# Kernel optimization log

Measured on AMD Instinct MI355X. Metric: run time of the kernel, lower is better.

The kernel has to match this reference:

```python
import math
import jax, jax.numpy as jnp
import numpy as np

N_HEADS = 16

def _alibi_slopes(n_heads: int) -> np.ndarray:
    def pow2_slopes(n):
        start = 2 ** (-2 ** (-(math.log2(n) - 3)))
        return [start * start ** i for i in range(n)]
    if math.log2(n_heads).is_integer():
        slopes = pow2_slopes(n_heads)
    else:
        closest = 2 ** math.floor(math.log2(n_heads))
        slopes = pow2_slopes(closest)
        extra = pow2_slopes(2 * closest)[0::2]
        slopes = slopes + extra[: n_heads - closest]
    return np.asarray(slopes, dtype=np.float32)

def _build_alibi_bias(n_heads: int, T: int) -> jnp.ndarray:
    # (1, H, T, T): lower triangle = -slope*|i-j|, strict upper = -inf (causal)
    slopes = jnp.asarray(_alibi_slopes(n_heads))  # (H,)
    pos = jnp.arange(T)
    dist = pos[None, :] - pos[None, :].T  # (T, T), j - i
    causal = dist < 0  # future positions (j > i means dist>0? note: dist = j - i transposed)
    # match torch: distances = positions[None,:] - positions[:,None] -> dist[i,j] = j - i
    dist = pos[None, :] - pos[:, None]
    causal = dist > 0  # wait: torch masks distances < 0 where distances[i,j] = j - i? No:
    # torch: distances = positions.unsqueeze(0) - positions.unsqueeze(1) -> dist[i,j] = positions[j] - positions[i]? 
    # unsqueeze(0): (1,T) row j; unsqueeze(1): (T,1) row i -> dist[i,j] = pos[j] - pos[i]
    # causal_mask = dist < 0 masks j < i ... but then bias upper triangle kept?
    # Actually torch masks where distances < 0, i.e., j < i (past). That seems inverted,
    # but we must be FAITHFUL: mask fills -inf where pos[j] - pos[i] < 0.
    d = pos[None, :] - pos[:, None]  # d[i,j] = j - i
    mask = d < 0
    bias = -slopes[:, None, None] * jnp.abs(d).astype(jnp.float32)[None, :, :]
    bias = jnp.where(mask[None, :, :], -jnp.inf, bias)
    return bias[None]  # (1, H, T, T)

def setup_inputs() -> dict:
    key = jax.random.key(0)
    k1, k2, k3 = jax.random.split(key, 3)
    B, T, D = 2, 2048, 1024
    x = jax.random.normal(k1, (B, T, D), dtype=jnp.float32)
    W_qkv = jax.random.normal(k2, (D, 3 * D), dtype=jnp.float32) * (1.0 / math.sqrt(D))
    W_out = jax.random.normal(k3, (D, D), dtype=jnp.float32) * (1.0 / math.sqrt(D))
    return {"x": x, "W_qkv": W_qkv, "W_out": W_out}

def reference(x, W_qkv, W_out):
    B, T, D = x.shape
    H = N_HEADS
    hd = D // H
    qkv = x @ W_qkv  # (B, T, 3D)
    q, k, v = jnp.split(qkv, 3, axis=-1)
    q = q.reshape(B, T, H, hd).transpose(0, 2, 1, 3)  # (B,H,T,hd)
    k = k.reshape(B, T, H, hd).transpose(0, 2, 1, 3)
    v = v.reshape(B, T, H, hd).transpose(0, 2, 1, 3)
    scale = 1.0 / math.sqrt(hd)
    attn = jnp.einsum('bhqd,bhkd->bhqk', q, k) * scale  # (B,H,T,T)
    attn = attn + _build_alibi_bias(H, T)
    attn = jax.nn.softmax(attn, axis=-1)
    out = jnp.einsum('bhqk,bhkd->bhqd', attn, v)  # (B,H,T,hd)
    out = out.transpose(0, 2, 1, 3).reshape(B, T, D)
    return out @ W_out
```

## Files before the change

kernel.cpp:

```cpp
#include <hip/hip_runtime.h>

#define DEV __device__ __forceinline__

typedef __attribute__((ext_vector_type(4))) float f32x4;
typedef __attribute__((ext_vector_type(16))) float f32x16;
typedef __attribute__((ext_vector_type(8))) short s16x8;

static constexpr int TB  = 2;
static constexpr int TT  = 2048;
static constexpr int TD  = 1024;
static constexpr int TH  = 16;
static constexpr int THD = 64;
static constexpr int TN3 = 3072;
static constexpr int TM  = TB * TT;

#define WS_FLAG   0u
#define WS_XB     1024u
#define WS_WQKVT  (WS_XB + 8388608u)
#define WS_WOUTT  (WS_WQKVT + 6291456u)
#define WS_QKV    (WS_WOUTT + 2097152u)
#define WS_VT     (WS_QKV + 25165824u)
#define WS_CTX    (WS_VT + 8388608u)

DEV unsigned short f2bf(float f) {
  unsigned int u = __builtin_bit_cast(unsigned int, f);
  u += 0x7FFFu + ((u >> 16) & 1u);
  return (unsigned short)(u >> 16);
}
DEV f32x4 mfma16(s16x8 a, s16x8 b, f32x4 c) {
  return __builtin_amdgcn_mfma_f32_16x16x32_bf16(a, b, c, 0, 0, 0);
}
DEV f32x16 mfma32(s16x8 a, s16x8 b, f32x16 c) {
  return __builtin_amdgcn_mfma_f32_32x32x16_bf16(a, b, c, 0, 0, 0);
}
DEV void gload_lds16(const void* g, void* l) {
  __builtin_amdgcn_global_load_lds(
      (const __attribute__((address_space(1))) void*)g,
      (__attribute__((address_space(3))) void*)l, 16, 0, 0);
}
DEV unsigned int cvtpk(float lo, float hi_) {
  unsigned int r;
  asm("v_cvt_pk_bf16_f32 %0, %1, %2" : "=v"(r) : "v"(lo), "v"(hi_));
  return r;
}
DEV void plswap(unsigned int& a, unsigned int& b) {
  asm("v_permlane32_swap_b32 %0, %1" : "+v"(a), "+v"(b));
}

__global__ __launch_bounds__(256) void detect_kernel(const uint4* __restrict__ probe,
                                                     int* __restrict__ flag) {
  __shared__ int cnt;
  if (threadIdx.x == 0) cnt = 0;
  __syncthreads();
  uint4 v = probe[threadIdx.x];
  int local = 0;
  unsigned int w[4] = {v.x, v.y, v.z, v.w};
#pragma unroll
  for (int k = 0; k < 4; ++k) {
    unsigned int e0 = (w[k] >> 7) & 0xFF;
    unsigned int e1 = (w[k] >> 23) & 0xFF;
    if (e0 >= 135) local++;
    if (e1 >= 135) local++;
  }
  atomicAdd(&cnt, local);
  __syncthreads();
  if (threadIdx.x == 0) flag[0] = (cnt < 100) ? 1 : 0;
}

__global__ __launch_bounds__(256) void prep_kernel(const void* __restrict__ x,
                                                   const void* __restrict__ wqkv,
                                                   const void* __restrict__ wout,
                                                   unsigned short* __restrict__ xb,
                                                   unsigned short* __restrict__ wqkvt,
                                                   unsigned short* __restrict__ woutt,
                                                   const int* __restrict__ flag) {
  __shared__ unsigned short tile[64 * 65];
  const int bid = blockIdx.x;
  const bool bf = (flag[0] != 0);
  if (bid < 1024) {
    const void* W; unsigned short* Wt; int N, k0, n0;
    if (bid < 768) { W = wqkv; Wt = wqkvt; N = TN3; k0 = (bid & 15) * 64; n0 = (bid >> 4) * 64; }
    else { int id = bid - 768; W = wout; Wt = woutt; N = TD; k0 = (id & 15) * 64; n0 = (id >> 4) * 64; }
    for (int e = threadIdx.x; e < 4096; e += 256) {
      int kr = e >> 6, nc = e & 63;
      unsigned short v;
      if (bf) v = ((const unsigned short*)W)[(size_t)(k0 + kr) * N + n0 + nc];
      else    v = f2bf(((const float*)W)[(size_t)(k0 + kr) * N + n0 + nc]);
      tile[kr * 65 + nc] = v;
    }
    __syncthreads();
    for (int e = threadIdx.x; e < 4096; e += 256) {
      int nr = e >> 6, kc = e & 63;
      Wt[(size_t)(n0 + nr) * TD + k0 + kc] = tile[kc * 65 + nr];
    }
  } else {
    if (bf) return;
    int i = (bid - 1024) * 256 + threadIdx.x;
    if (i >= (TM * TD) / 8) return;
    const float* s = (const float*)x + (size_t)i * 8;
    unsigned int w0 = (unsigned int)f2bf(s[0]) | ((unsigned int)f2bf(s[1]) << 16);
    unsigned int w1 = (unsigned int)f2bf(s[2]) | ((unsigned int)f2bf(s[3]) << 16);
    unsigned int w2 = (unsigned int)f2bf(s[4]) | ((unsigned int)f2bf(s[5]) << 16);
    unsigned int w3 = (unsigned int)f2bf(s[6]) | ((unsigned int)f2bf(s[7]) << 16);
    uint4 o; o.x = w0; o.y = w1; o.z = w2; o.w = w3;
    ((uint4*)xb)[i] = o;
  }
}

__global__ __launch_bounds__(512, 4) void gemm_8p_kernel(const unsigned short* __restrict__ Axb,
                                                         const unsigned short* __restrict__ xraw,
                                                         const unsigned short* __restrict__ Bt,
                                                         unsigned short* __restrict__ C,
                                                         unsigned short* __restrict__ vtb,
                                                         int Mn, int Nn, int Kn,
                                                         const int* __restrict__ flag) {
  __shared__ unsigned short lA[2][128 * 64];
  __shared__ unsigned short lB[2][192 * 64];
  const int tid = threadIdx.x;
  const int lane = tid & 63;
  const int wid = tid >> 6;
  const int wm = wid >> 2, wn = wid & 3;
  const int l15 = lane & 15, lg = lane >> 4;

  const int nby = Nn / 192;
  const int nwg = (Mn >> 7) * nby;
  const int cpx = nwg >> 3;
  const int bid = blockIdx.x;
  const int swz = (bid & 7) * cpx + (bid >> 3);
  const int bm = swz / nby, bn = swz % nby;
  const int row0 = bm << 7, col0 = bn * 192;

  const unsigned short* Abase = flag[0] ? xraw : Axb;

  const int srow = tid >> 3;
  const int scol = ((tid & 7) ^ (srow & 7)) * 8;
  const unsigned short* aS = Abase + (size_t)(row0 + srow) * Kn + scol;
  const unsigned short* bS = Bt + (size_t)(col0 + srow) * Kn + scol;
  const size_t r64 = (size_t)64 * Kn;

#define STGA(dst, koff) do {                                \
    unsigned short* _d = (dst) + tid * 8;                   \
    const unsigned short* _s = aS + (koff);                 \
    gload_lds16(_s,       _d);                              \
    gload_lds16(_s + r64, _d + 4096);                       \
  } while (0)
#define STGB(dst, koff) do {                                \
    unsigned short* _d = (dst) + tid * 8;                   \
    const unsigned short* _s = bS + (koff);                 \
    gload_lds16(_s,           _d);                          \
    gload_lds16(_s + r64,     _d + 4096);                   \
    gload_lds16(_s + 2 * r64, _d + 8192);                   \
  } while (0)

  f32x4 acc[4][3];
#pragma unroll
  for (int m = 0; m < 4; ++m)
#pragma unroll
    for (int n = 0; n < 3; ++n) acc[m][n] = (f32x4){0.f, 0.f, 0.f, 0.f};

  const int sa = l15 & 7;
  const int kc0 = (lg ^ sa) * 8;
  const int kc1 = ((4 + lg) ^ sa) * 8;
  const int aRow = (wm * 64 + l15) * 64;
  const int bRow = (wn * 48 + l15) * 64;

  STGA(&lA[0][0], 0);
  STGB(&lB[0][0], 0);
  asm volatile("s_waitcnt vmcnt(0)" ::: "memory");
  __builtin_amdgcn_s_barrier();

  const int nt = Kn >> 6;
  for (int t = 0; t < nt; ++t) {
    const unsigned short* la = &lA[t & 1][0];
    const unsigned short* lb = &lB[t & 1][0];
    unsigned short* na = &lA[(t + 1) & 1][0];
    unsigned short* nb = &lB[(t + 1) & 1][0];
    const int koff = (t + 1) << 6;
    const bool more = (t + 1 < nt);

    if (more) { STGA(na, koff); STGB(nb, koff); }

    s16x8 a0[4], a1[4], b0[3], b1[3];
#pragma unroll
    for (int m = 0; m < 4; ++m) {
      a0[m] = *(const s16x8*)&la[aRow + m * 1024 + kc0];
      a1[m] = *(const s16x8*)&la[aRow + m * 1024 + kc1];
    }
#pragma unroll
    for (int n = 0; n < 3; ++n) {
      b0[n] = *(const s16x8*)&lb[bRow + n * 1024 + kc0];
      b1[n] = *(const s16x8*)&lb[bRow + n * 1024 + kc1];
    }
#pragma unroll
    for (int m = 0; m < 4; ++m)
#pragma unroll
      for (int n = 0; n < 3; ++n) {
        acc[m][n] = mfma16(a0[m], b0[n], acc[m][n]);
        acc[m][n] = mfma16(a1[m], b1[n], acc[m][n]);
      }

    asm volatile("s_waitcnt vmcnt(0)" ::: "memory");
    __builtin_amdgcn_s_barrier();
  }
#undef STGA
#undef STGB

  unsigned short* cw = C + (size_t)(row0 + wm * 64 + lg * 4) * Nn + col0 + wn * 48 + l15;
#pragma unroll
  for (int m = 0; m < 4; ++m)
#pragma unroll
    for (int n = 0; n < 3; ++n) {
      const int cbase = col0 + wn * 48 + n * 16;
      if (cbase < 2048) {
#pragma unroll
        for (int j = 0; j < 4; ++j)
          cw[(size_t)(m * 16 + j) * Nn + n * 16] = f2bf(acc[m][n][j]);
      } else {
        int tg = row0 + wm * 64 + lg * 4 + m * 16;
        int bb = tg >> 11, tt = tg & 2047;
        int cc2 = cbase + l15 - 2048;
        int h = cc2 >> 6, d = cc2 & 63;
        unsigned short* dst = vtb + (((size_t)(bb * 16 + h) * 64 + d) << 11) + tt;
        uint2 pk;
        pk.x = cvtpk(acc[m][n][0], acc[m][n][1]);
        pk.y = cvtpk(acc[m][n][2], acc[m][n][3]);
        *(uint2*)dst = pk;
      }
    }
}

__global__ __launch_bounds__(256, 2) void gemm_bt2_kernel(const unsigned short* __restrict__ A,
                                                          const unsigned short* __restrict__ Bt,
                                                          void* __restrict__ Cout,
                                                          int Mn, int Nn, int Kn,
                                                          const int* __restrict__ flag) {
  __shared__ unsigned short lA[3][128 * 64];
  __shared__ unsigned short lB[3][64 * 64];
  const int tid  = threadIdx.x;
  const int lane = tid & 63, wid = tid >> 6;
  const int wr = wid >> 1, wc = wid & 1;
  const int l15 = lane & 15, lg = lane >> 4;
  const int row0 = blockIdx.x * 128, col0 = blockIdx.y * 64;

  f32x4 acc[4][2];
#pragma unroll
  for (int m = 0; m < 4; ++m)
#pragma unroll
    for (int n = 0; n < 2; ++n) acc[m][n] = (f32x4){0.f, 0.f, 0.f, 0.f};

  const int srow = tid >> 3;
  const int scol = ((tid & 7) ^ (srow & 7)) * 8;
  const unsigned short* aS = A  + (size_t)(row0 + srow) * Kn + scol;
  const unsigned short* bS = Bt + (size_t)(col0 + srow) * Kn + scol;
  const size_t r32 = (size_t)32 * Kn;

#define STG2(bi, koff) do {                                                 \
    unsigned short* _da = &lA[bi][0] + tid * 8;                             \
    unsigned short* _db = &lB[bi][0] + tid * 8;                             \
    gload_lds16(aS + (koff),            _da);                               \
    gload_lds16(aS + (koff) + r32,      _da + 2048);                        \
    gload_lds16(aS + (koff) + 2 * r32,  _da + 4096);                        \
    gload_lds16(aS + (koff) + 3 * r32,  _da + 6144);                        \
    gload_lds16(bS + (koff),            _db);                               \
    gload_lds16(bS + (koff) + r32,      _db + 2048);                        \
  } while (0)

  const int sa = l15 & 7;
  const int kc0 = (lg ^ sa) * 8;
  const int kc1 = ((4 + lg) ^ sa) * 8;
  const int aoff = (wr * 64 + l15) * 64;
  const int boff = (wc * 32 + l15) * 64;

  const int nt = Kn >> 6;
  STG2(0, 0);
  STG2(1, 64);
  asm volatile("s_waitcnt vmcnt(6)" ::: "memory");
  __builtin_amdgcn_s_barrier();

  int cur = 0;
  for (int t = 0; t < nt; ++t) {
    const unsigned short* la = &lA[cur][0];
    const unsigned short* lb = &lB[cur][0];
    const bool deep = (t + 2 < nt);

    s16x8 af[4], bfv[2];
#pragma unroll
    for (int m = 0; m < 4; ++m) af[m] = *(const s16x8*)&la[aoff + m * 1024 + kc0];
#pragma unroll
    for (int n = 0; n < 2; ++n) bfv[n] = *(const s16x8*)&lb[boff + n * 1024 + kc0];
    if (deep) { int nbuf = (cur + 2 == 3) ? 0 : ((cur + 2 == 4) ? 1 : cur + 2); STG2(nbuf, (t + 2) << 6); }
    __builtin_amdgcn_s_barrier();
    asm volatile("s_waitcnt lgkmcnt(0)" ::: "memory");
    __builtin_amdgcn_sched_barrier(0);
    __builtin_amdgcn_s_setprio(1);
#pragma unroll
    for (int m = 0; m < 4; ++m)
#pragma unroll
      for (int n = 0; n < 2; ++n)
        acc[m][n] = mfma16(af[m], bfv[n], acc[m][n]);
    __builtin_amdgcn_s_setprio(0);
    __builtin_amdgcn_s_barrier();

#pragma unroll
    for (int m = 0; m < 4; ++m) af[m] = *(const s16x8*)&la[aoff + m * 1024 + kc1];
#pragma unroll
    for (int n = 0; n < 2; ++n) bfv[n] = *(const s16x8*)&lb[boff + n * 1024 + kc1];
    __builtin_amdgcn_s_barrier();
    asm volatile("s_waitcnt lgkmcnt(0)" ::: "memory");
    __builtin_amdgcn_sched_barrier(0);
    __builtin_amdgcn_s_setprio(1);
#pragma unroll
    for (int m = 0; m < 4; ++m)
#pragma unroll
      for (int n = 0; n < 2; ++n)
        acc[m][n] = mfma16(af[m], bfv[n], acc[m][n]);
    __builtin_amdgcn_s_setprio(0);
    if (t + 1 < nt) {
      if (deep) asm volatile("s_waitcnt vmcnt(6)" ::: "memory");
      else      asm volatile("s_waitcnt vmcnt(0)" ::: "memory");
      __builtin_amdgcn_s_barrier();
    }
    cur = (cur == 2) ? 0 : cur + 1;
  }
#undef STG2

  const bool obf = (flag[0] != 0);
#pragma unroll
  for (int m = 0; m < 4; ++m)
#pragma unroll
    for (int n = 0; n < 2; ++n)
#pragma unroll
      for (int j = 0; j < 4; ++j) {
        int r = row0 + wr * 64 + m * 16 + lg * 4 + j;
        int c = col0 + wc * 32 + n * 16 + l15;
        if (obf) ((unsigned short*)Cout)[(size_t)r * Nn + c] = f2bf(acc[m][n][j]);
        else     ((float*)Cout)[(size_t)r * Nn + c] = acc[m][n][j];
      }
}

__global__ __launch_bounds__(256, 4) void attn_kernel(const unsigned short* __restrict__ qkv,
                                                      const unsigned short* __restrict__ vt,
                                                      unsigned short* __restrict__ ctx) {
  __shared__ __align__(16) unsigned char smem[32768];
  unsigned short* kl0 = (unsigned short*)smem;
  unsigned short* vl0 = (unsigned short*)(smem + 16384);
  float* red = (float*)smem;

  const int bid = blockIdx.x;
  const int r_ = bid & 255, q_ = bid >> 8;
  const int s_ = r_ >> 5, g_ = r_ & 31;
  const int bh = (g_ + 8 * q_) & 31;
  const int x32 = (q_ == 0) ? s_ : (q_ == 1) ? 15 - s_ : (q_ == 2) ? 16 + s_ : 31 - s_;
  const int b = bh >> 4, h = bh & 15;

  const int tid = threadIdx.x;
  const int wid = tid >> 6, lane = tid & 63;
  const int wr = wid & 1, wk = wid >> 1;
  const int l31 = lane & 31, hi = lane >> 5;
  const int i_base = x32 * 64 + wr * 32;

  const unsigned short* qb  = qkv + (size_t)b * TT * TN3 + h * THD;
  const unsigned short* kb_ = qkv + (size_t)b * TT * TN3 + TD + h * THD;
  const unsigned short* vb_ = vt + (size_t)bh * THD * TT;

  const float LOG2E = 1.44269504f;
  const float SL2 = exp2f(-0.5f * (float)(h + 1)) * LOG2E;
  const float SC2 = 0.125f * LOG2E;
  const float dbias = -SL2 * 64.0f;

  const int t_rel = (int)((140.0f / SL2 + 63.0f) * (1.0f / 64.0f)) + 1;
  const int t_end = (32 < x32 + t_rel) ? 32 : x32 + t_rel;

  const int srow = tid >> 3;
  const int sx = ((tid & 7) ^ (srow & 7)) * 8;
  const unsigned short* srcK = kb_ + (size_t)(x32 * 64 + srow) * TN3 + sx;
  const unsigned short* srcV = vb_ + (size_t)srow * TT + x32 * 64 + sx;
  const size_t kstep = (size_t)64 * TN3;

#define STAGE(bufi) do {                                   \
    unsigned short* _dk = kl0 + (bufi) * 4096 + tid * 8;   \
    unsigned short* _dv = vl0 + (bufi) * 4096 + tid * 8;   \
    gload_lds16(srcK,            _dk);                     \
    gload_lds16(srcK + 32 * TN3, _dk + 2048);              \
    gload_lds16(srcV,            _dv);                     \
    gload_lds16(srcV + 32 * TT,  _dv + 2048);              \
  } while (0)

  s16x8 qa[4];
  {
    const unsigned short* qr = qb + (size_t)(i_base + l31) * TN3 + hi * 8;
#pragma unroll
    for (int dd = 0; dd < 4; ++dd) qa[dd] = *(const s16x8*)(qr + dd * 16);
  }

  s16x8 ones;
  {
    short ov = (l31 == 0) ? (short)0x3F80 : (short)0;
#pragma unroll
    for (int e = 0; e < 8; ++e) ones[e] = ov;
  }

  float base[16];
#pragma unroll
  for (int r = 0; r < 16; ++r) {
    int cr0 = (r & 3) + 8 * (r >> 2);
    base[r] = -SL2 * (float)(wk * 32 + cr0 + 4 * hi - wr * 32 - l31) - 16.0f;
  }

  f32x16 o0, o1, ol;
#pragma unroll
  for (int r = 0; r < 16; ++r) { o0[r] = 0.f; o1[r] = 0.f; ol[r] = 0.f; }

  const int sw = (l31 & 7) << 4;
  int cc[4];
#pragma unroll
  for (int dd = 0; dd < 4; ++dd) cc[dd] = ((dd * 32 + hi * 16) ^ sw) >> 1;

  int cur = 0;
  STAGE(0); srcK += kstep; srcV += 64;
  asm volatile("s_waitcnt vmcnt(0)" ::: "memory");
  __syncthreads();

  for (int t = x32; t < t_end; ++t) {
    if (t + 1 < t_end) { STAGE(cur ^ 1); srcK += kstep; srcV += 64; }

    const unsigned short* kb = kl0 + cur * 4096;
    const unsigned short* vbl = vl0 + cur * 4096;

    f32x16 sv;
#pragma unroll
    for (int r = 0; r < 16; ++r) sv[r] = 0.f;
    __builtin_amdgcn_s_setprio(1);
#pragma unroll
    for (int dd = 0; dd < 4; ++dd) {
      s16x8 k0 = *(const s16x8*)&kb[(wk * 32 + l31) * 64 + cc[dd]];
      sv = mfma32(k0, qa[dd], sv);
    }
    __builtin_amdgcn_s_setprio(0);

    if (t == x32) {
#pragma unroll
      for (int r = 0; r < 16; ++r) {
        float bb = base[r];
        float v = __builtin_amdgcn_exp2f(fmaf(sv[r], SC2, bb));
        sv[r] = (bb > -15.999f) ? 0.0f : v;
      }
    } else {
#pragma unroll
      for (int r = 0; r < 16; ++r)
        sv[r] = __builtin_amdgcn_exp2f(fmaf(sv[r], SC2, base[r]));
    }
#pragma unroll
    for (int r = 0; r < 16; ++r) base[r] += dbias;

    s16x8 pa[2];
#pragma unroll
    for (int mh = 0; mh < 2; ++mh) {
      unsigned int a0 = cvtpk(sv[8 * mh + 0], sv[8 * mh + 1]);
      unsigned int a1 = cvtpk(sv[8 * mh + 2], sv[8 * mh + 3]);
      unsigned int b0 = cvtpk(sv[8 * mh + 4], sv[8 * mh + 5]);
      unsigned int b1 = cvtpk(sv[8 * mh + 6], sv[8 * mh + 7]);
      plswap(a0, b0); plswap(a1, b1);
      uint4 u; u.x = a0; u.y = a1; u.z = b0; u.w = b1;
      pa[mh] = __builtin_bit_cast(s16x8, u);
    }

    __builtin_amdgcn_s_setprio(1);
#pragma unroll
    for (int ks = 0; ks < 2; ++ks) {
      s16x8 v0 = *(const s16x8*)&vbl[l31 * 64 + cc[wk * 2 + ks]];
      s16x8 v1 = *(const s16x8*)&vbl[(32 + l31) * 64 + cc[wk * 2 + ks]];
      o0 = mfma32(pa[ks], v0, o0);
      o1 = mfma32(pa[ks], v1, o1);
      ol = mfma32(pa[ks], ones, ol);
    }
    __builtin_amdgcn_s_setprio(0);

    asm volatile("s_waitcnt vmcnt(0)" ::: "memory");
    __syncthreads();
    cur ^= 1;
  }
#undef STAGE

  const int rbase = (wr * 64 + lane) * 49;
  if (wk == 1) {
#pragma unroll
    for (int r = 0; r < 16; ++r) red[rbase + r] = o0[r];
#pragma unroll
    for (int r = 0; r < 16; ++r) red[rbase + 16 + r] = o1[r];
#pragma unroll
    for (int r = 0; r < 16; ++r) red[rbase + 32 + r] = ol[r];
  }
  __syncthreads();
  if (wk == 0) {
#pragma unroll
    for (int r = 0; r < 16; ++r) o0[r] += red[rbase + r];
#pragma unroll
    for (int r = 0; r < 16; ++r) o1[r] += red[rbase + 16 + r];
#pragma unroll
    for (int r = 0; r < 16; ++r) ol[r] += red[rbase + 32 + r];

    float rdiv[16];
#pragma unroll
    for (int r = 0; r < 16; ++r) rdiv[r] = 1.0f / __shfl(ol[r], lane & 32);

    unsigned short* cb = ctx + (size_t)(b * TT + i_base) * TD + h * THD + l31;
#pragma unroll
    for (int r = 0; r < 16; ++r) {
      int row = (r & 3) + 8 * (r >> 2) + 4 * hi;
      unsigned int pk = cvtpk(o0[r] * rdiv[r], o1[r] * rdiv[r]);
      cb[(size_t)row * TD] = (unsigned short)pk;
      cb[(size_t)row * TD + 32] = (unsigned short)(pk >> 16);
    }
  }
}

extern "C" void kernel_launch(void* const* d_in, const int* in_sizes, int n_in,
                              void* d_out, int out_size, void* d_ws, size_t ws_size,
                              hipStream_t stream) {
  const void* x    = d_in[0];
  const void* wqkv = d_in[1];
  const void* wout = d_in[2];
  char* ws = (char*)d_ws;
  int* flag             = (int*)(ws + WS_FLAG);
  unsigned short* xb    = (unsigned short*)(ws + WS_XB);
  unsigned short* wqkvt = (unsigned short*)(ws + WS_WQKVT);
  unsigned short* woutt = (unsigned short*)(ws + WS_WOUTT);
  unsigned short* qkvb  = (unsigned short*)(ws + WS_QKV);
  unsigned short* vtb   = (unsigned short*)(ws + WS_VT);
  unsigned short* ctxb  = (unsigned short*)(ws + WS_CTX);

  detect_kernel<<<1, 256, 0, stream>>>((const uint4*)x, flag);
  prep_kernel<<<3072, 256, 0, stream>>>(x, wqkv, wout, xb, wqkvt, woutt, flag);
  gemm_8p_kernel<<<(TM / 128) * (TN3 / 192), 512, 0, stream>>>(xb, (const unsigned short*)x, wqkvt, qkvb, vtb, TM, TN3, TD, flag);
  attn_kernel<<<1024, 256, 0, stream>>>(qkvb, vtb, ctxb);
  gemm_bt2_kernel<<<dim3(TM / 128, TD / 64), 256, 0, stream>>>(ctxb, woutt, d_out, TM, TD, TD, flag);
}
```

Baseline: 102.4 us.

## Switch QKV GEMM to 32x32 MFMA with 4 waves and inline dtype detection

The QKV projection GEMM moves from 8 waves issuing 16x16x32 MFMAs to 4 waves issuing 32x32x16 MFMAs, so each wave computes a 64x96 tile. The aim is fewer LDS fragment reads per FLOP and higher MFMA throughput. The separate detect kernel and its global flag are removed: each kernel now checks the input dtype itself with a wave ballot over the first 64 uint4 of x, which saves one launch. The cost is higher register pressure per wave (launch bounds 256,2) and a smaller probe sample for the dtype heuristic.

```diff
diff --git a/kernel.cpp b/kernel.cpp
--- a/kernel.cpp
+++ b/kernel.cpp
@@ -14,7 +14,6 @@
 static constexpr int TN3 = 3072;
 static constexpr int TM  = TB * TT;
 
-#define WS_FLAG   0u
 #define WS_XB     1024u
 #define WS_WQKVT  (WS_XB + 8388608u)
 #define WS_WOUTT  (WS_WQKVT + 6291456u)
@@ -47,24 +46,16 @@
   asm("v_permlane32_swap_b32 %0, %1" : "+v"(a), "+v"(b));
 }
 
-__global__ __launch_bounds__(256) void detect_kernel(const uint4* __restrict__ probe,
-                                                     int* __restrict__ flag) {
-  __shared__ int cnt;
-  if (threadIdx.x == 0) cnt = 0;
-  __syncthreads();
-  uint4 v = probe[threadIdx.x];
-  int local = 0;
+DEV bool is_bf16(const void* x) {
+  uint4 v = ((const uint4*)x)[threadIdx.x & 63];
   unsigned int w[4] = {v.x, v.y, v.z, v.w};
+  int hit = 0;
 #pragma unroll
   for (int k = 0; k < 4; ++k) {
-    unsigned int e0 = (w[k] >> 7) & 0xFF;
-    unsigned int e1 = (w[k] >> 23) & 0xFF;
-    if (e0 >= 135) local++;
-    if (e1 >= 135) local++;
-  }
-  atomicAdd(&cnt, local);
-  __syncthreads();
-  if (threadIdx.x == 0) flag[0] = (cnt < 100) ? 1 : 0;
+    if (((w[k] >> 7) & 0xFF) >= 135) hit++;
+    if (((w[k] >> 23) & 0xFF) >= 135) hit++;
+  }
+  return __ballot(hit > 0) == 0ULL;
 }
 
 __global__ __launch_bounds__(256) void prep_kernel(const void* __restrict__ x,
@@ -72,11 +63,10 @@
                                                    const void* __restrict__ wout,
                                                    unsigned short* __restrict__ xb,
                                                    unsigned short* __restrict__ wqkvt,
-                                                   unsigned short* __restrict__ woutt,
-                                                   const int* __restrict__ flag) {
+                                                   unsigned short* __restrict__ woutt) {
   __shared__ unsigned short tile[64 * 65];
   const int bid = blockIdx.x;
-  const bool bf = (flag[0] != 0);
+  const bool bf = is_bf16(x);
   if (bid < 1024) {
     const void* W; unsigned short* Wt; int N, k0, n0;
     if (bid < 768) { W = wqkv; Wt = wqkvt; N = TN3; k0 = (bid & 15) * 64; n0 = (bid >> 4) * 64; }
@@ -107,20 +97,19 @@
   }
 }
 
-__global__ __launch_bounds__(512, 4) void gemm_8p_kernel(const unsigned short* __restrict__ Axb,
-                                                         const unsigned short* __restrict__ xraw,
-                                                         const unsigned short* __restrict__ Bt,
-                                                         unsigned short* __restrict__ C,
-                                                         unsigned short* __restrict__ vtb,
-                                                         int Mn, int Nn, int Kn,
-                                                         const int* __restrict__ flag) {
+__global__ __launch_bounds__(256, 2) void gemm1_kernel(const unsigned short* __restrict__ Axb,
+                                                       const unsigned short* __restrict__ xraw,
+                                                       const unsigned short* __restrict__ Bt,
+                                                       unsigned short* __restrict__ C,
+                                                       unsigned short* __restrict__ vtb,
+                                                       int Mn, int Nn, int Kn) {
   __shared__ unsigned short lA[2][128 * 64];
   __shared__ unsigned short lB[2][192 * 64];
   const int tid = threadIdx.x;
   const int lane = tid & 63;
   const int wid = tid >> 6;
-  const int wm = wid >> 2, wn = wid & 3;
-  const int l15 = lane & 15, lg = lane >> 4;
+  const int wm = wid >> 1, wn = wid & 1;
+  const int l31 = lane & 31, hi = lane >> 5;
 
   const int nby = Nn / 192;
   const int nwg = (Mn >> 7) * nby;
@@ -130,39 +119,47 @@
   const int bm = swz / nby, bn = swz % nby;
   const int row0 = bm << 7, col0 = bn * 192;
 
-  const unsigned short* Abase = flag[0] ? xraw : Axb;
+  const bool bf = is_bf16(xraw);
+  const unsigned short* Abase = bf ? xraw : Axb;
 
   const int srow = tid >> 3;
   const int scol = ((tid & 7) ^ (srow & 7)) * 8;
   const unsigned short* aS = Abase + (size_t)(row0 + srow) * Kn + scol;
   const unsigned short* bS = Bt + (size_t)(col0 + srow) * Kn + scol;
-  const size_t r64 = (size_t)64 * Kn;
+  const size_t r32 = (size_t)32 * Kn;
 
 #define STGA(dst, koff) do {                                \
     unsigned short* _d = (dst) + tid * 8;                   \
     const unsigned short* _s = aS + (koff);                 \
-    gload_lds16(_s,       _d);                              \
-    gload_lds16(_s + r64, _d + 4096);                       \
+    gload_lds16(_s,           _d);                          \
+    gload_lds16(_s + r32,     _d + 2048);                   \
+    gload_lds16(_s + 2 * r32, _d + 4096);                   \
+    gload_lds16(_s + 3 * r32, _d + 6144);                   \
   } while (0)
 #define STGB(dst, koff) do {                                \
     unsigned short* _d = (dst) + tid * 8;                   \
     const unsigned short* _s = bS + (koff);                 \
     gload_lds16(_s,           _d);                          \
-    gload_lds16(_s + r64,     _d + 4096);                   \
-    gload_lds16(_s + 2 * r64, _d + 8192);                   \
+    gload_lds16(_s + r32,     _d + 2048);                   \
+    gload_lds16(_s + 2 * r32, _d + 4096);                   \
+    gload_lds16(_s + 3 * r32, _d + 6144);                   \
+    gload_lds16(_s + 4 * r32, _d + 8192);                   \
+    gload_lds16(_s + 5 * r32, _d + 10240);                  \
   } while (0)
 
-  f32x4 acc[4][3];
-#pragma unroll
-  for (int m = 0; m < 4; ++m)
-#pragma unroll
-    for (int n = 0; n < 3; ++n) acc[m][n] = (f32x4){0.f, 0.f, 0.f, 0.f};
-
-  const int sa = l15 & 7;
-  const int kc0 = (lg ^ sa) * 8;
-  const int kc1 = ((4 + lg) ^ sa) * 8;
-  const int aRow = (wm * 64 + l15) * 64;
-  const int bRow = (wn * 48 + l15) * 64;
+  f32x16 acc[2][3];
+#pragma unroll
+  for (int m = 0; m < 2; ++m)
+#pragma unroll
+    for (int n = 0; n < 3; ++n)
+#pragma unroll
+      for (int r = 0; r < 16; ++r) acc[m][n][r] = 0.f;
+
+  int kcc[4];
+#pragma unroll
+  for (int ks = 0; ks < 4; ++ks) kcc[ks] = ((ks * 2 + hi) ^ (l31 & 7)) * 8;
+  const int aRow = (wm * 64 + l31) * 64;
+  const int bRow = (wn * 96 + l31) * 64;
 
   STGA(&lA[0][0], 0);
   STGB(&lB[0][0], 0);
@@ -180,24 +177,24 @@
 
     if (more) { STGA(na, koff); STGB(nb, koff); }
 
-    s16x8 a0[4], a1[4], b0[3], b1[3];
-#pragma unroll
-    for (int m = 0; m < 4; ++m) {
-      a0[m] = *(const s16x8*)&la[aRow + m * 1024 + kc0];
-      a1[m] = *(const s16x8*)&la[aRow + m * 1024 + kc1];
-    }
-#pragma unroll
-    for (int n = 0; n < 3; ++n) {
-      b0[n] = *(const s16x8*)&lb[bRow + n * 1024 + kc0];
-      b1[n] = *(const s16x8*)&lb[bRow + n * 1024 + kc1];
-    }
-#pragma unroll
-    for (int m = 0; m < 4; ++m)
-#pragma unroll
-      for (int n = 0; n < 3; ++n) {
-        acc[m][n] = mfma16(a0[m], b0[n], acc[m][n]);
-        acc[m][n] = mfma16(a1[m], b1[n], acc[m][n]);
-      }
+    s16x8 xa[2][4], yb[3][4];
+#pragma unroll
+    for (int m = 0; m < 2; ++m)
+#pragma unroll
+      for (int ks = 0; ks < 4; ++ks)
+        xa[m][ks] = *(const s16x8*)&la[aRow + m * 2048 + kcc[ks]];
+#pragma unroll
+    for (int n = 0; n < 3; ++n)
+#pragma unroll
+      for (int ks = 0; ks < 4; ++ks)
+        yb[n][ks] = *(const s16x8*)&lb[bRow + n * 2048 + kcc[ks]];
+#pragma unroll
+    for (int ks = 0; ks < 4; ++ks)
+#pragma unroll
+      for (int m = 0; m < 2; ++m)
+#pragma unroll
+        for (int n = 0; n < 3; ++n)
+          acc[m][n] = mfma32(xa[m][ks], yb[n][ks], acc[m][n]);
 
     asm volatile("s_waitcnt vmcnt(0)" ::: "memory");
     __builtin_amdgcn_s_barrier();
@@ -205,26 +202,31 @@
 #undef STGA
 #undef STGB
 
-  unsigned short* cw = C + (size_t)(row0 + wm * 64 + lg * 4) * Nn + col0 + wn * 48 + l15;
-#pragma unroll
-  for (int m = 0; m < 4; ++m)
+  unsigned short* cw = C + (size_t)(row0 + wm * 64 + 4 * hi) * Nn + col0 + wn * 96 + l31;
+#pragma unroll
+  for (int m = 0; m < 2; ++m)
 #pragma unroll
     for (int n = 0; n < 3; ++n) {
-      const int cbase = col0 + wn * 48 + n * 16;
+      const int cbase = col0 + wn * 96 + n * 32;
       if (cbase < 2048) {
 #pragma unroll
-        for (int j = 0; j < 4; ++j)
-          cw[(size_t)(m * 16 + j) * Nn + n * 16] = f2bf(acc[m][n][j]);
+        for (int r = 0; r < 16; ++r) {
+          int rr = (r & 3) + 8 * (r >> 2);
+          cw[(size_t)(m * 32 + rr) * Nn + n * 32] = f2bf(acc[m][n][r]);
+        }
       } else {
-        int tg = row0 + wm * 64 + lg * 4 + m * 16;
-        int bb = tg >> 11, tt = tg & 2047;
-        int cc2 = cbase + l15 - 2048;
+        int cc2 = cbase + l31 - 2048;
         int h = cc2 >> 6, d = cc2 & 63;
-        unsigned short* dst = vtb + (((size_t)(bb * 16 + h) * 64 + d) << 11) + tt;
-        uint2 pk;
-        pk.x = cvtpk(acc[m][n][0], acc[m][n][1]);
-        pk.y = cvtpk(acc[m][n][2], acc[m][n][3]);
-        *(uint2*)dst = pk;
+#pragma unroll
+        for (int g = 0; g < 4; ++g) {
+          int tg = row0 + wm * 64 + m * 32 + 8 * g + 4 * hi;
+          int bb = tg >> 11, tt = tg & 2047;
+          unsigned short* dst = vtb + (((size_t)(bb * 16 + h) * 64 + d) << 11) + tt;
+          uint2 pk;
+          pk.x = cvtpk(acc[m][n][4 * g + 0], acc[m][n][4 * g + 1]);
+          pk.y = cvtpk(acc[m][n][4 * g + 2], acc[m][n][4 * g + 3]);
+          *(uint2*)dst = pk;
+        }
       }
     }
 }
@@ -233,7 +235,7 @@
                                                           const unsigned short* __restrict__ Bt,
                                                           void* __restrict__ Cout,
                                                           int Mn, int Nn, int Kn,
-                                                          const int* __restrict__ flag) {
+                                                          const unsigned short* __restrict__ xprobe) {
   __shared__ unsigned short lA[3][128 * 64];
   __shared__ unsigned short lB[3][64 * 64];
   const int tid  = threadIdx.x;
@@ -241,6 +243,8 @@
   const int wr = wid >> 1, wc = wid & 1;
   const int l15 = lane & 15, lg = lane >> 4;
   const int row0 = blockIdx.x * 128, col0 = blockIdx.y * 64;
+
+  const bool obf = is_bf16(xprobe);
 
   f32x4 acc[4][2];
 #pragma unroll
@@ -324,7 +328,6 @@
   }
 #undef STG2
 
-  const bool obf = (flag[0] != 0);
 #pragma unroll
   for (int m = 0; m < 4; ++m)
 #pragma unroll
@@ -522,7 +525,6 @@
   const void* wqkv = d_in[1];
   const void* wout = d_in[2];
   char* ws = (char*)d_ws;
-  int* flag             = (int*)(ws + WS_FLAG);
   unsigned short* xb    = (unsigned short*)(ws + WS_XB);
   unsigned short* wqkvt = (unsigned short*)(ws + WS_WQKVT);
   unsigned short* woutt = (unsigned short*)(ws + WS_WOUTT);
@@ -530,9 +532,8 @@
   unsigned short* vtb   = (unsigned short*)(ws + WS_VT);
   unsigned short* ctxb  = (unsigned short*)(ws + WS_CTX);
 
-  detect_kernel<<<1, 256, 0, stream>>>((const uint4*)x, flag);
-  prep_kernel<<<3072, 256, 0, stream>>>(x, wqkv, wout, xb, wqkvt, woutt, flag);
-  gemm_8p_kernel<<<(TM / 128) * (TN3 / 192), 512, 0, stream>>>(xb, (const unsigned short*)x, wqkvt, qkvb, vtb, TM, TN3, TD, flag);
+  prep_kernel<<<3072, 256, 0, stream>>>(x, wqkv, wout, xb, wqkvt, woutt);
+  gemm1_kernel<<<(TM / 128) * (TN3 / 192), 256, 0, stream>>>(xb, (const unsigned short*)x, wqkvt, qkvb, vtb, TM, TN3, TD);
   attn_kernel<<<1024, 256, 0, stream>>>(qkvb, vtb, ctxb);
-  gemm_bt2_kernel<<<dim3(TM / 128, TD / 64), 256, 0, stream>>>(ctxb, woutt, d_out, TM, TD, TD, flag);
-}
+  gemm_bt2_kernel<<<dim3(TM / 128, TD / 64), 256, 0, stream>>>(ctxb, woutt, d_out, TM, TD, TD, (const unsigned short*)x);
+}
```

New measurement: 102.8 us. No clear change (+0.4%).
